# Optimization experiments

Hardware: AMD Instinct MI355X
Metric: run time of the kernel (lower is better)

## Reference

```python
import jax, jax.numpy as jnp
import numpy as np

N = 8192
D = 128
NUM_CLASSES = 1000
MARGIN = 1.0
EPS = 1e-6  # torch.nn.functional.pairwise_distance default eps
FMAX = float(np.finfo(np.float32).max)


def setup_inputs() -> dict:
    key = jax.random.key(0)
    k_e, k_l = jax.random.split(key)
    embed = jax.random.normal(k_e, (N, D), dtype=jnp.float32)
    labels = jax.random.randint(k_l, (N,), 0, NUM_CLASSES, dtype=jnp.int64)
    return {"embed": embed, "labels": labels}


def reference(embed, labels):
    # Pairwise squared-L2 distance matrix: ||xi||^2 - 2 xi.xj + ||xj||^2  -> [N, N]
    norm_sq = jnp.sum(embed * embed, axis=1, keepdims=True)  # [N, 1]
    dist = norm_sq - 2.0 * (embed @ embed.T) + norm_sq.T     # [N, N]

    # Label similarity mask (int in original; float here for the multiplies)
    sim = (labels[:, None] == labels[None, :]).astype(dist.dtype)  # [N, N]

    # Hardest positive: argmax of masked distances
    hardest_pos = jnp.argmax(dist * sim, axis=1)  # [N]

    # Hardest negative: argmin over negatives, sentinel-replacing masked-out entries
    neg_masked = dist * (1.0 - sim)
    hardest_neg = jnp.argmin(neg_masked + (neg_masked <= 0).astype(dist.dtype) * FMAX, axis=1)

    a = embed
    p = embed[hardest_pos]  # [N, D]
    n = embed[hardest_neg]  # [N, D]

    # torch.nn.TripletMarginLoss(margin=MARGIN): mean(relu(d(a,p) - d(a,n) + margin))
    # with d(x, y) = ||x - y + eps||_2 (torch pairwise_distance semantics)
    d_ap = jnp.sqrt(jnp.sum((a - p + EPS) ** 2, axis=1))
    d_an = jnp.sqrt(jnp.sum((a - n + EPS) ** 2, axis=1))
    loss = jnp.mean(jnp.maximum(d_ap - d_an + MARGIN, 0.0))
    return loss
```

## Files before the change

### kernel.cpp

```cpp
#include <hip/hip_runtime.h>
#include <cstdint>

typedef unsigned long long u64;
typedef _Float16 half8 __attribute__((ext_vector_type(8)));
typedef float f32x4 __attribute__((ext_vector_type(4)));

static constexpr int Dd = 128;
static constexpr float EPSf = 1e-6f;
static constexpr float MARGINf = 1.0f;
static constexpr float BIGf = 3.0e38f;

__device__ __forceinline__ unsigned fkey(float f) {
  unsigned b = __float_as_uint(f);
  return (b & 0x80000000u) ? ~b : (b | 0x80000000u);
}

__global__ __launch_bounds__(256) void k_prep(const float* __restrict__ E,
                                              const int* __restrict__ lab,
                                              _Float16* __restrict__ Eh,
                                              float2* __restrict__ nl,
                                              u64* __restrict__ posPack,
                                              u64* __restrict__ negPack) {
  int row = (blockIdx.x * 256 + threadIdx.x) >> 6;
  int l = threadIdx.x & 63;
  float2 v = *(const float2*)(E + row * Dd + l * 2);
  union { _Float16 h[2]; unsigned u; } cv;
  cv.h[0] = (_Float16)v.x;
  cv.h[1] = (_Float16)v.y;
  *(unsigned*)(Eh + row * Dd + l * 2) = cv.u;
  float s = v.x * v.x + v.y * v.y;
  #pragma unroll
  for (int off = 32; off; off >>= 1) s += __shfl_xor(s, off);
  if (l == 0) {
    float2 q;
    q.x = s;
    q.y = __int_as_float(lab[row]);
    nl[row] = q;
    posPack[row] = 0ull;
    negPack[row] = ~0ull;
  }
}

__global__ __launch_bounds__(512, 2) void k_gemm(const _Float16* __restrict__ Eh,
                                                 const float2* __restrict__ nl,
                                                 const int* __restrict__ lab,
                                                 u64* __restrict__ posPack,
                                                 u64* __restrict__ negPack) {
  __shared__ __align__(1024) _Float16 As[256 * 128];
  __shared__ __align__(1024) _Float16 Bs[256 * 128];
  __shared__ __align__(16) float2 nlj[256];

  const int t = threadIdx.x;
  const int w = t >> 6, l = t & 63;
  const int jbase = (blockIdx.x >> 5) * 256;
  const int ibase = (blockIdx.x & 31) * 256;
  const int lane15 = l & 15, lg = l >> 4;
  const int iw = w & 3, jw = w >> 2;

  {
    const int cp = lane15 << 4;
    #pragma unroll
    for (int ci = 0; ci < 16; ++ci) {
      int chunk = w * 16 + ci;
      int r = (chunk & 63) * 4 + lg;
      int gbase = (chunk < 64) ? jbase : ibase;
      _Float16* tile = (chunk < 64) ? As : Bs;
      half8 v = *(const half8*)((const char*)Eh + (size_t)(gbase + r) * 256 + cp);
      *(half8*)((char*)tile + r * 256 + (cp ^ ((r & 7) << 4))) = v;
    }
    if (t < 256) nlj[t] = nl[jbase + t];
  }

  int li[4];
  #pragma unroll
  for (int it = 0; it < 4; ++it) li[it] = lab[ibase + iw * 64 + it * 16 + lane15];

  __syncthreads();

  f32x4 acc[8][4];
  #pragma unroll
  for (int a = 0; a < 8; ++a)
    #pragma unroll
    for (int b = 0; b < 4; ++b) acc[a][b] = (f32x4){0.f, 0.f, 0.f, 0.f};

  #pragma unroll
  for (int ks = 0; ks < 4; ++ks) {
    const int bc = ks * 64 + lg * 16;
    half8 af[8], bf[4];
    #pragma unroll
    for (int jt = 0; jt < 8; ++jt) {
      int r = jw * 128 + jt * 16 + lane15;
      af[jt] = *(const half8*)((const char*)As + r * 256 + (bc ^ ((r & 7) << 4)));
    }
    #pragma unroll
    for (int it = 0; it < 4; ++it) {
      int r = iw * 64 + it * 16 + lane15;
      bf[it] = *(const half8*)((const char*)Bs + r * 256 + (bc ^ ((r & 7) << 4)));
    }
    #pragma unroll
    for (int jt = 0; jt < 8; ++jt)
      #pragma unroll
      for (int it = 0; it < 4; ++it)
        acc[jt][it] = __builtin_amdgcn_mfma_f32_16x16x32_f16(af[jt], bf[it], acc[jt][it], 0, 0, 0);
  }

  float bp[4], bn[4];
  #pragma unroll
  for (int it = 0; it < 4; ++it) { bp[it] = -BIGf; bn[it] = BIGf; }

  #pragma unroll
  for (int jt = 0; jt < 8; ++jt) {
    const int jr0 = jw * 128 + jt * 16 + lg * 4;
    float4 q01 = *(const float4*)(nlj + jr0);
    float4 q23 = *(const float4*)(nlj + jr0 + 2);
    float nj[4] = {q01.x, q01.z, q23.x, q23.z};
    int ljv[4] = {__float_as_int(q01.y), __float_as_int(q01.w),
                  __float_as_int(q23.y), __float_as_int(q23.w)};
    #pragma unroll
    for (int it = 0; it < 4; ++it) {
      float pc[4], nc[4];
      #pragma unroll
      for (int r = 0; r < 4; ++r) {
        float d = fmaf(acc[jt][it][r], -2.0f, nj[r]);
        float dv = __uint_as_float((__float_as_uint(d) & 0xFFFFFF00u) |
                                   (unsigned)(jr0 + r));
        bool sim = (ljv[r] == li[it]);
        pc[r] = sim ? dv : -BIGf;
        nc[r] = sim ? BIGf : dv;
      }
      bp[it] = fmaxf(bp[it], fmaxf(fmaxf(pc[0], pc[1]), fmaxf(pc[2], pc[3])));
      bn[it] = fminf(bn[it], fminf(fminf(nc[0], nc[1]), fminf(nc[2], nc[3])));
    }
  }

  #pragma unroll
  for (int it = 0; it < 4; ++it) {
    #pragma unroll
    for (int s = 16; s < 64; s <<= 1) {
      bp[it] = fmaxf(bp[it], __shfl_xor(bp[it], s));
      bn[it] = fminf(bn[it], __shfl_xor(bn[it], s));
    }
  }
  if (l < 16) {
    #pragma unroll
    for (int it = 0; it < 4; ++it) {
      int gi = ibase + iw * 64 + it * 16 + lane15;
      int jp = jbase + (int)(__float_as_uint(bp[it]) & 255u);
      int jn = jbase + (int)(__float_as_uint(bn[it]) & 255u);
      atomicMax(posPack + gi, ((u64)fkey(bp[it]) << 32) | (u64)(0xFFFFFFFFu - (unsigned)jp));
      atomicMin(negPack + gi, ((u64)fkey(bn[it]) << 32) | (u64)(unsigned)jn);
    }
  }
}

__global__ __launch_bounds__(256) void k_final(const float* __restrict__ E,
                                               const u64* __restrict__ posPack,
                                               const u64* __restrict__ negPack,
                                               float* __restrict__ rowLoss) {
  int i = (blockIdx.x * 256 + threadIdx.x) >> 6;
  int l = threadIdx.x & 63;
  int jp = (int)(0xFFFFFFFFu - (unsigned)(posPack[i] & 0xFFFFFFFFull));
  int jn = (int)(unsigned)(negPack[i] & 0xFFFFFFFFull);
  float2 a = *(const float2*)(E + i * Dd + l * 2);
  float2 p = *(const float2*)(E + jp * Dd + l * 2);
  float2 n = *(const float2*)(E + jn * Dd + l * 2);
  float dx = a.x - p.x + EPSf, dy = a.y - p.y + EPSf;
  float sap = dx * dx + dy * dy;
  dx = a.x - n.x + EPSf;
  dy = a.y - n.y + EPSf;
  float san = dx * dx + dy * dy;
  #pragma unroll
  for (int off = 32; off; off >>= 1) {
    sap += __shfl_xor(sap, off);
    san += __shfl_xor(san, off);
  }
  if (l == 0) rowLoss[i] = fmaxf(sqrtf(sap) - sqrtf(san) + MARGINf, 0.0f);
}

__global__ __launch_bounds__(256) void k_reduce(const float* __restrict__ rowLoss,
                                                float* __restrict__ out) {
  __shared__ float s[256];
  int t = threadIdx.x;
  float sum = 0.f;
  for (int q = 0; q < 32; ++q) sum += rowLoss[t + 256 * q];
  s[t] = sum;
  __syncthreads();
  for (int off = 128; off; off >>= 1) {
    if (t < off) s[t] += s[t + off];
    __syncthreads();
  }
  if (t == 0) out[0] = s[0] * (1.0f / 8192.0f);
}

extern "C" void kernel_launch(void* const* d_in, const int* in_sizes, int n_in,
                              void* d_out, int out_size, void* d_ws, size_t ws_size,
                              hipStream_t stream) {
  const float* E = (const float*)d_in[0];
  const int* lab = (const int*)d_in[1];
  float* out = (float*)d_out;

  char* wsp = (char*)d_ws;
  u64* posPack = (u64*)wsp;
  u64* negPack = (u64*)(wsp + (64 << 10));
  float2* nl = (float2*)(wsp + (128 << 10));
  float* rowLoss = (float*)(wsp + (192 << 10));
  _Float16* Eh = (_Float16*)(wsp + (256 << 10));

  k_prep<<<2048, 256, 0, stream>>>(E, lab, Eh, nl, posPack, negPack);
  k_gemm<<<1024, 512, 0, stream>>>(Eh, nl, lab, posPack, negPack);
  k_final<<<2048, 256, 0, stream>>>(E, posPack, negPack, rowLoss);
  k_reduce<<<1, 256, 0, stream>>>(rowLoss, out);
}
```

Baseline: 49.14 us.

## Stream j-tiles with double-buffered direct-to-LDS loads and drop global atomics

The GEMM kernel now assigns each block a 128-row i-tile against a 1024-column j-strip. The i fragments stay in registers while four 256-row j-tiles are streamed through double-buffered LDS using global_load_lds, so the next tile's loads overlap the current tile's MFMAs. Per-block argmax/argmin results go to per-strip partial arrays instead of 64-bit atomics, and the final kernel reduces over the 8 strips. This cuts LDS staging cost and atomic contention, at the price of fewer blocks (512) and a larger workspace. The distance value now keeps fewer mantissa bits because 10 bits are used to hold the column index.

```diff
diff --git a/kernel.cpp b/kernel.cpp
--- a/kernel.cpp
+++ b/kernel.cpp
@@ -15,12 +15,16 @@
   return (b & 0x80000000u) ? ~b : (b | 0x80000000u);
 }
 
+__device__ __forceinline__ void gl_lds16(const void* g, void* l) {
+  __builtin_amdgcn_global_load_lds(
+      (const __attribute__((address_space(1))) unsigned int*)g,
+      (__attribute__((address_space(3))) unsigned int*)l, 16, 0, 0);
+}
+
 __global__ __launch_bounds__(256) void k_prep(const float* __restrict__ E,
                                               const int* __restrict__ lab,
                                               _Float16* __restrict__ Eh,
-                                              float2* __restrict__ nl,
-                                              u64* __restrict__ posPack,
-                                              u64* __restrict__ negPack) {
+                                              float2* __restrict__ nl) {
   int row = (blockIdx.x * 256 + threadIdx.x) >> 6;
   int l = threadIdx.x & 63;
   float2 v = *(const float2*)(E + row * Dd + l * 2);
@@ -36,101 +40,133 @@
     q.x = s;
     q.y = __int_as_float(lab[row]);
     nl[row] = q;
-    posPack[row] = 0ull;
-    negPack[row] = ~0ull;
   }
 }
 
 __global__ __launch_bounds__(512, 2) void k_gemm(const _Float16* __restrict__ Eh,
                                                  const float2* __restrict__ nl,
                                                  const int* __restrict__ lab,
-                                                 u64* __restrict__ posPack,
-                                                 u64* __restrict__ negPack) {
-  __shared__ __align__(1024) _Float16 As[256 * 128];
-  __shared__ __align__(1024) _Float16 Bs[256 * 128];
-  __shared__ __align__(16) float2 nlj[256];
+                                                 u64* __restrict__ posPart,
+                                                 u64* __restrict__ negPart) {
+  __shared__ __align__(16) _Float16 jA[2][256 * 128];
+  __shared__ __align__(16) float2 jNL[2][256];
+  __shared__ float sc[2][4][128];
 
   const int t = threadIdx.x;
   const int w = t >> 6, l = t & 63;
-  const int jbase = (blockIdx.x >> 5) * 256;
-  const int ibase = (blockIdx.x & 31) * 256;
   const int lane15 = l & 15, lg = l >> 4;
-  const int iw = w & 3, jw = w >> 2;
-
-  {
-    const int cp = lane15 << 4;
-    #pragma unroll
-    for (int ci = 0; ci < 16; ++ci) {
-      int chunk = w * 16 + ci;
-      int r = (chunk & 63) * 4 + lg;
-      int gbase = (chunk < 64) ? jbase : ibase;
-      _Float16* tile = (chunk < 64) ? As : Bs;
-      half8 v = *(const half8*)((const char*)Eh + (size_t)(gbase + r) * 256 + cp);
-      *(half8*)((char*)tile + r * 256 + (cp ^ ((r & 7) << 4))) = v;
-    }
-    if (t < 256) nlj[t] = nl[jbase + t];
-  }
+  const int ig = w & 1, jw = w >> 1;
+  const int ip = blockIdx.x & 63, js = blockIdx.x >> 6;
+  const int ibase = ip * 128;
+  const int jbase = js * 1024;
+
+  #pragma unroll
+  for (int qi = 0; qi < 4; ++qi) {
+    int q = w * 4 + qi;
+    int row = q * 4 + lg;
+    gl_lds16((const char*)Eh + (size_t)(ibase + row) * 256 + ((lane15 << 4) ^ ((row & 7) << 4)),
+             (char*)&jA[0][0] + q * 1024);
+  }
+  #pragma unroll
+  for (int qi = 0; qi < 8; ++qi) {
+    int q = w * 8 + qi;
+    int row = q * 4 + lg;
+    gl_lds16((const char*)Eh + (size_t)(jbase + row) * 256 + ((lane15 << 4) ^ ((row & 7) << 4)),
+             (char*)&jA[1][0] + q * 1024);
+  }
+  if (w < 2)
+    gl_lds16((const char*)nl + (size_t)jbase * 8 + w * 1024 + l * 16,
+             (char*)&jNL[1][0] + w * 1024);
 
   int li[4];
   #pragma unroll
-  for (int it = 0; it < 4; ++it) li[it] = lab[ibase + iw * 64 + it * 16 + lane15];
-
-  __syncthreads();
-
-  f32x4 acc[8][4];
-  #pragma unroll
-  for (int a = 0; a < 8; ++a)
-    #pragma unroll
-    for (int b = 0; b < 4; ++b) acc[a][b] = (f32x4){0.f, 0.f, 0.f, 0.f};
-
-  #pragma unroll
-  for (int ks = 0; ks < 4; ++ks) {
-    const int bc = ks * 64 + lg * 16;
-    half8 af[8], bf[4];
-    #pragma unroll
-    for (int jt = 0; jt < 8; ++jt) {
-      int r = jw * 128 + jt * 16 + lane15;
-      af[jt] = *(const half8*)((const char*)As + r * 256 + (bc ^ ((r & 7) << 4)));
-    }
-    #pragma unroll
-    for (int it = 0; it < 4; ++it) {
-      int r = iw * 64 + it * 16 + lane15;
-      bf[it] = *(const half8*)((const char*)Bs + r * 256 + (bc ^ ((r & 7) << 4)));
-    }
-    #pragma unroll
-    for (int jt = 0; jt < 8; ++jt)
-      #pragma unroll
-      for (int it = 0; it < 4; ++it)
-        acc[jt][it] = __builtin_amdgcn_mfma_f32_16x16x32_f16(af[jt], bf[it], acc[jt][it], 0, 0, 0);
-  }
+  for (int it = 0; it < 4; ++it) li[it] = lab[ibase + ig * 64 + it * 16 + lane15];
+
+  __syncthreads();
+
+  half8 bf[4][4];
+  #pragma unroll
+  for (int it = 0; it < 4; ++it) {
+    #pragma unroll
+    for (int ks = 0; ks < 4; ++ks) {
+      int r = ig * 64 + it * 16 + lane15;
+      int bc = ks * 64 + lg * 16;
+      bf[it][ks] = *(const half8*)((const char*)&jA[0][0] + r * 256 + (bc ^ ((r & 7) << 4)));
+    }
+  }
+  __syncthreads();
 
   float bp[4], bn[4];
   #pragma unroll
   for (int it = 0; it < 4; ++it) { bp[it] = -BIGf; bn[it] = BIGf; }
 
   #pragma unroll
-  for (int jt = 0; jt < 8; ++jt) {
-    const int jr0 = jw * 128 + jt * 16 + lg * 4;
-    float4 q01 = *(const float4*)(nlj + jr0);
-    float4 q23 = *(const float4*)(nlj + jr0 + 2);
-    float nj[4] = {q01.x, q01.z, q23.x, q23.z};
-    int ljv[4] = {__float_as_int(q01.y), __float_as_int(q01.w),
-                  __float_as_int(q23.y), __float_as_int(q23.w)};
-    #pragma unroll
-    for (int it = 0; it < 4; ++it) {
-      float pc[4], nc[4];
-      #pragma unroll
-      for (int r = 0; r < 4; ++r) {
-        float d = fmaf(acc[jt][it][r], -2.0f, nj[r]);
-        float dv = __uint_as_float((__float_as_uint(d) & 0xFFFFFF00u) |
-                                   (unsigned)(jr0 + r));
-        bool sim = (ljv[r] == li[it]);
-        pc[r] = sim ? dv : -BIGf;
-        nc[r] = sim ? BIGf : dv;
+  for (int tt = 0; tt < 4; ++tt) {
+    const int cur = 1 - (tt & 1);
+    const int nxt = tt & 1;
+
+    if (tt < 3) {
+      const int jr = jbase + (tt + 1) * 256;
+      #pragma unroll
+      for (int qi = 0; qi < 8; ++qi) {
+        int q = w * 8 + qi;
+        int row = q * 4 + lg;
+        gl_lds16((const char*)Eh + (size_t)(jr + row) * 256 + ((lane15 << 4) ^ ((row & 7) << 4)),
+                 (char*)&jA[nxt][0] + q * 1024);
       }
-      bp[it] = fmaxf(bp[it], fmaxf(fmaxf(pc[0], pc[1]), fmaxf(pc[2], pc[3])));
-      bn[it] = fminf(bn[it], fminf(fminf(nc[0], nc[1]), fminf(nc[2], nc[3])));
-    }
+      if (w < 2)
+        gl_lds16((const char*)nl + (size_t)jr * 8 + w * 1024 + l * 16,
+                 (char*)&jNL[nxt][0] + w * 1024);
+    }
+
+    f32x4 acc[4][4];
+    #pragma unroll
+    for (int a = 0; a < 4; ++a)
+      #pragma unroll
+      for (int b = 0; b < 4; ++b) acc[a][b] = (f32x4){0.f, 0.f, 0.f, 0.f};
+
+    #pragma unroll
+    for (int ks = 0; ks < 4; ++ks) {
+      const int bc = ks * 64 + lg * 16;
+      half8 af[4];
+      #pragma unroll
+      for (int jt = 0; jt < 4; ++jt) {
+        int r = jw * 64 + jt * 16 + lane15;
+        af[jt] = *(const half8*)((const char*)&jA[cur][0] + r * 256 + (bc ^ ((r & 7) << 4)));
+      }
+      #pragma unroll
+      for (int jt = 0; jt < 4; ++jt)
+        #pragma unroll
+        for (int it = 0; it < 4; ++it)
+          acc[jt][it] = __builtin_amdgcn_mfma_f32_16x16x32_f16(af[jt], bf[it][ks], acc[jt][it], 0, 0, 0);
+    }
+
+    const unsigned tb = (unsigned)(tt * 256 + jw * 64 + lg * 4);
+    #pragma unroll
+    for (int jt = 0; jt < 4; ++jt) {
+      const int jr0 = jw * 64 + jt * 16 + lg * 4;
+      float4 q01 = *(const float4*)&jNL[cur][jr0];
+      float4 q23 = *(const float4*)&jNL[cur][jr0 + 2];
+      const float njv[4] = {q01.x, q01.z, q23.x, q23.z};
+      const int ljv[4] = {__float_as_int(q01.y), __float_as_int(q01.w),
+                          __float_as_int(q23.y), __float_as_int(q23.w)};
+      const unsigned ib = tb + (unsigned)(jt * 16);
+      #pragma unroll
+      for (int it = 0; it < 4; ++it) {
+        float pcv[4], ncv[4];
+        #pragma unroll
+        for (int r = 0; r < 4; ++r) {
+          float d = fmaf(acc[jt][it][r], -2.0f, njv[r]);
+          float dv = __uint_as_float((__float_as_uint(d) & 0xFFFFFC00u) | (ib + (unsigned)r));
+          bool sim = (ljv[r] == li[it]);
+          pcv[r] = sim ? dv : -BIGf;
+          ncv[r] = sim ? BIGf : dv;
+        }
+        bp[it] = fmaxf(bp[it], fmaxf(fmaxf(pcv[0], pcv[1]), fmaxf(pcv[2], pcv[3])));
+        bn[it] = fminf(bn[it], fminf(fminf(ncv[0], ncv[1]), fminf(ncv[2], ncv[3])));
+      }
+    }
+    __syncthreads();
   }
 
   #pragma unroll
@@ -144,23 +180,39 @@
   if (l < 16) {
     #pragma unroll
     for (int it = 0; it < 4; ++it) {
-      int gi = ibase + iw * 64 + it * 16 + lane15;
-      int jp = jbase + (int)(__float_as_uint(bp[it]) & 255u);
-      int jn = jbase + (int)(__float_as_uint(bn[it]) & 255u);
-      atomicMax(posPack + gi, ((u64)fkey(bp[it]) << 32) | (u64)(0xFFFFFFFFu - (unsigned)jp));
-      atomicMin(negPack + gi, ((u64)fkey(bn[it]) << 32) | (u64)(unsigned)jn);
-    }
+      sc[0][jw][ig * 64 + it * 16 + lane15] = bp[it];
+      sc[1][jw][ig * 64 + it * 16 + lane15] = bn[it];
+    }
+  }
+  __syncthreads();
+
+  if (t < 128) {
+    float p = fmaxf(fmaxf(sc[0][0][t], sc[0][1][t]), fmaxf(sc[0][2][t], sc[0][3][t]));
+    float n = fminf(fminf(sc[1][0][t], sc[1][1][t]), fminf(sc[1][2][t], sc[1][3][t]));
+    unsigned jp = (unsigned)jbase + (__float_as_uint(p) & 1023u);
+    unsigned jn = (unsigned)jbase + (__float_as_uint(n) & 1023u);
+    posPart[(size_t)js * 8192 + ibase + t] =
+        ((u64)fkey(p) << 32) | (u64)(0xFFFFFFFFu - jp);
+    negPart[(size_t)js * 8192 + ibase + t] = ((u64)fkey(n) << 32) | (u64)jn;
   }
 }
 
 __global__ __launch_bounds__(256) void k_final(const float* __restrict__ E,
-                                               const u64* __restrict__ posPack,
-                                               const u64* __restrict__ negPack,
+                                               const u64* __restrict__ posPart,
+                                               const u64* __restrict__ negPart,
                                                float* __restrict__ rowLoss) {
   int i = (blockIdx.x * 256 + threadIdx.x) >> 6;
   int l = threadIdx.x & 63;
-  int jp = (int)(0xFFFFFFFFu - (unsigned)(posPack[i] & 0xFFFFFFFFull));
-  int jn = (int)(unsigned)(negPack[i] & 0xFFFFFFFFull);
+  u64 pp = 0ull, np = ~0ull;
+  #pragma unroll
+  for (int s = 0; s < 8; ++s) {
+    u64 a = posPart[(size_t)s * 8192 + i];
+    u64 b = negPart[(size_t)s * 8192 + i];
+    pp = pp > a ? pp : a;
+    np = np < b ? np : b;
+  }
+  int jp = (int)(0xFFFFFFFFu - (unsigned)(pp & 0xFFFFFFFFull));
+  int jn = (int)(unsigned)(np & 0xFFFFFFFFull);
   float2 a = *(const float2*)(E + i * Dd + l * 2);
   float2 p = *(const float2*)(E + jp * Dd + l * 2);
   float2 n = *(const float2*)(E + jn * Dd + l * 2);
@@ -200,14 +252,14 @@
   float* out = (float*)d_out;
 
   char* wsp = (char*)d_ws;
-  u64* posPack = (u64*)wsp;
-  u64* negPack = (u64*)(wsp + (64 << 10));
-  float2* nl = (float2*)(wsp + (128 << 10));
-  float* rowLoss = (float*)(wsp + (192 << 10));
-  _Float16* Eh = (_Float16*)(wsp + (256 << 10));
-
-  k_prep<<<2048, 256, 0, stream>>>(E, lab, Eh, nl, posPack, negPack);
-  k_gemm<<<1024, 512, 0, stream>>>(Eh, nl, lab, posPack, negPack);
-  k_final<<<2048, 256, 0, stream>>>(E, posPack, negPack, rowLoss);
+  u64* posPart = (u64*)wsp;
+  u64* negPart = (u64*)(wsp + (512 << 10));
+  float2* nl = (float2*)(wsp + (1024 << 10));
+  float* rowLoss = (float*)(wsp + (1088 << 10));
+  _Float16* Eh = (_Float16*)(wsp + (1152 << 10));
+
+  k_prep<<<2048, 256, 0, stream>>>(E, lab, Eh, nl);
+  k_gemm<<<512, 512, 0, stream>>>(Eh, nl, lab, posPart, negPart);
+  k_final<<<2048, 256, 0, stream>>>(E, posPart, negPart, rowLoss);
   k_reduce<<<1, 256, 0, stream>>>(rowLoss, out);
 }
```

Measured after the change: 48.06 us. 1.02x faster.

## Pre-pack fp16 embeddings in MFMA fragment layout and shrink GEMM tiles to 128x128

Applied to the files above, without the earlier changes.

The prep kernel now writes the fp16 embeddings in a layout that matches the MFMA fragment order, so the GEMM can copy tiles to LDS linearly and read fragments without the XOR swizzle. The GEMM block tile drops from 256x256 with 512 threads to 128x128 with 256 threads, which gives four times as many blocks and fewer accumulators per wave. It also raises wave priority around the MFMA sequence. The cost is more redundant tile loads across blocks and more atomic updates, and the packed index now keeps only 7 low bits, which slightly changes how near-tied distances are broken.

```diff
diff --git a/kernel.cpp b/kernel.cpp
--- a/kernel.cpp
+++ b/kernel.cpp
@@ -16,139 +16,140 @@
 }
 
 __global__ __launch_bounds__(256) void k_prep(const float* __restrict__ E,
-                                              const int* __restrict__ lab,
-                                              _Float16* __restrict__ Eh,
-                                              float2* __restrict__ nl,
+                                              _Float16* __restrict__ Ehp,
+                                              float* __restrict__ normf,
                                               u64* __restrict__ posPack,
                                               u64* __restrict__ negPack) {
-  int row = (blockIdx.x * 256 + threadIdx.x) >> 6;
-  int l = threadIdx.x & 63;
-  float2 v = *(const float2*)(E + row * Dd + l * 2);
-  union { _Float16 h[2]; unsigned u; } cv;
-  cv.h[0] = (_Float16)v.x;
-  cv.h[1] = (_Float16)v.y;
-  *(unsigned*)(Eh + row * Dd + l * 2) = cv.u;
-  float s = v.x * v.x + v.y * v.y;
-  #pragma unroll
-  for (int off = 32; off; off >>= 1) s += __shfl_xor(s, off);
-  if (l == 0) {
-    float2 q;
-    q.x = s;
-    q.y = __int_as_float(lab[row]);
-    nl[row] = q;
+  __shared__ float part[4][16];
+  const int t = threadIdx.x;
+  const int b = blockIdx.x;
+  const int ks = t >> 6, r15 = t & 15;
+  const int lg = (t >> 4) & 3;
+  const float* src = E + (size_t)(b * 16 + r15) * Dd + ks * 32 + lg * 8;
+  float4 v0 = *(const float4*)src;
+  float4 v1 = *(const float4*)(src + 4);
+  half8 hv;
+  hv[0] = (_Float16)v0.x; hv[1] = (_Float16)v0.y;
+  hv[2] = (_Float16)v0.z; hv[3] = (_Float16)v0.w;
+  hv[4] = (_Float16)v1.x; hv[5] = (_Float16)v1.y;
+  hv[6] = (_Float16)v1.z; hv[7] = (_Float16)v1.w;
+  *(half8*)((char*)Ehp + (size_t)b * 4096 + t * 16) = hv;
+  float s = v0.x * v0.x + v0.y * v0.y + v0.z * v0.z + v0.w * v0.w +
+            v1.x * v1.x + v1.y * v1.y + v1.z * v1.z + v1.w * v1.w;
+  s += __shfl_xor(s, 16);
+  s += __shfl_xor(s, 32);
+  if (((t >> 4) & 3) == 0) part[ks][r15] = s;
+  __syncthreads();
+  if (t < 16) {
+    int row = b * 16 + t;
+    normf[row] = part[0][t] + part[1][t] + part[2][t] + part[3][t];
     posPack[row] = 0ull;
     negPack[row] = ~0ull;
   }
 }
 
-__global__ __launch_bounds__(512, 2) void k_gemm(const _Float16* __restrict__ Eh,
-                                                 const float2* __restrict__ nl,
+__global__ __launch_bounds__(256, 2) void k_gemm(const _Float16* __restrict__ Ehp,
+                                                 const float* __restrict__ normf,
                                                  const int* __restrict__ lab,
                                                  u64* __restrict__ posPack,
                                                  u64* __restrict__ negPack) {
-  __shared__ __align__(1024) _Float16 As[256 * 128];
-  __shared__ __align__(1024) _Float16 Bs[256 * 128];
-  __shared__ __align__(16) float2 nlj[256];
+  __shared__ __align__(16) char As[32768];
+  __shared__ __align__(16) char Bs[32768];
+  __shared__ __align__(16) float njs[128];
+  __shared__ __align__(16) int ljs[128];
 
   const int t = threadIdx.x;
   const int w = t >> 6, l = t & 63;
-  const int jbase = (blockIdx.x >> 5) * 256;
-  const int ibase = (blockIdx.x & 31) * 256;
   const int lane15 = l & 15, lg = l >> 4;
-  const int iw = w & 3, jw = w >> 2;
-
-  {
-    const int cp = lane15 << 4;
-    #pragma unroll
-    for (int ci = 0; ci < 16; ++ci) {
-      int chunk = w * 16 + ci;
-      int r = (chunk & 63) * 4 + lg;
-      int gbase = (chunk < 64) ? jbase : ibase;
-      _Float16* tile = (chunk < 64) ? As : Bs;
-      half8 v = *(const half8*)((const char*)Eh + (size_t)(gbase + r) * 256 + cp);
-      *(half8*)((char*)tile + r * 256 + (cp ^ ((r & 7) << 4))) = v;
-    }
-    if (t < 256) nlj[t] = nl[jbase + t];
-  }
-
+  const int iw = w & 1, jw = w >> 1;
+  const int ibase = (blockIdx.x & 63) * 128;
+  const int jbase = (blockIdx.x >> 6) * 128;
+  const char* jsrc = (const char*)Ehp + (size_t)(jbase >> 4) * 4096;
+  const char* isrc = (const char*)Ehp + (size_t)(ibase >> 4) * 4096;
+
+  #pragma unroll
+  for (int p = 0; p < 8; ++p)
+    *(half8*)(As + p * 4096 + t * 16) = *(const half8*)(jsrc + p * 4096 + t * 16);
+  #pragma unroll
+  for (int p = 0; p < 8; ++p)
+    *(half8*)(Bs + p * 4096 + t * 16) = *(const half8*)(isrc + p * 4096 + t * 16);
+  if (t < 128) {
+    njs[t] = normf[jbase + t];
+    ljs[t] = lab[jbase + t];
+  }
   int li[4];
   #pragma unroll
   for (int it = 0; it < 4; ++it) li[it] = lab[ibase + iw * 64 + it * 16 + lane15];
-
   __syncthreads();
 
-  f32x4 acc[8][4];
-  #pragma unroll
-  for (int a = 0; a < 8; ++a)
+  f32x4 acc[4][4];
+  #pragma unroll
+  for (int a = 0; a < 4; ++a)
     #pragma unroll
     for (int b = 0; b < 4; ++b) acc[a][b] = (f32x4){0.f, 0.f, 0.f, 0.f};
 
   #pragma unroll
   for (int ks = 0; ks < 4; ++ks) {
-    const int bc = ks * 64 + lg * 16;
-    half8 af[8], bf[4];
-    #pragma unroll
-    for (int jt = 0; jt < 8; ++jt) {
-      int r = jw * 128 + jt * 16 + lane15;
-      af[jt] = *(const half8*)((const char*)As + r * 256 + (bc ^ ((r & 7) << 4)));
-    }
-    #pragma unroll
-    for (int it = 0; it < 4; ++it) {
-      int r = iw * 64 + it * 16 + lane15;
-      bf[it] = *(const half8*)((const char*)Bs + r * 256 + (bc ^ ((r & 7) << 4)));
-    }
-    #pragma unroll
-    for (int jt = 0; jt < 8; ++jt)
+    half8 af[4], bf[4];
+    #pragma unroll
+    for (int jt = 0; jt < 4; ++jt)
+      af[jt] = *(const half8*)(As + ((jw * 4 + jt) * 4 + ks) * 1024 + l * 16);
+    #pragma unroll
+    for (int it = 0; it < 4; ++it)
+      bf[it] = *(const half8*)(Bs + ((iw * 4 + it) * 4 + ks) * 1024 + l * 16);
+    __builtin_amdgcn_s_setprio(1);
+    #pragma unroll
+    for (int jt = 0; jt < 4; ++jt)
       #pragma unroll
       for (int it = 0; it < 4; ++it)
         acc[jt][it] = __builtin_amdgcn_mfma_f32_16x16x32_f16(af[jt], bf[it], acc[jt][it], 0, 0, 0);
-  }
-
-  float bp[4], bn[4];
-  #pragma unroll
-  for (int it = 0; it < 4; ++it) { bp[it] = -BIGf; bn[it] = BIGf; }
-
-  #pragma unroll
-  for (int jt = 0; jt < 8; ++jt) {
-    const int jr0 = jw * 128 + jt * 16 + lg * 4;
-    float4 q01 = *(const float4*)(nlj + jr0);
-    float4 q23 = *(const float4*)(nlj + jr0 + 2);
-    float nj[4] = {q01.x, q01.z, q23.x, q23.z};
-    int ljv[4] = {__float_as_int(q01.y), __float_as_int(q01.w),
-                  __float_as_int(q23.y), __float_as_int(q23.w)};
+    __builtin_amdgcn_s_setprio(0);
+  }
+
+  float bp[4] = {-BIGf, -BIGf, -BIGf, -BIGf};
+  float bn[4] = {BIGf, BIGf, BIGf, BIGf};
+
+  #pragma unroll
+  for (int jt = 0; jt < 4; ++jt) {
+    const int jr0 = jw * 64 + jt * 16 + lg * 4;
+    const float4 nj4 = *(const float4*)&njs[jr0];
+    const int4 lj4 = *(const int4*)&ljs[jr0];
     #pragma unroll
     for (int it = 0; it < 4; ++it) {
-      float pc[4], nc[4];
-      #pragma unroll
-      for (int r = 0; r < 4; ++r) {
-        float d = fmaf(acc[jt][it][r], -2.0f, nj[r]);
-        float dv = __uint_as_float((__float_as_uint(d) & 0xFFFFFF00u) |
-                                   (unsigned)(jr0 + r));
-        bool sim = (ljv[r] == li[it]);
-        pc[r] = sim ? dv : -BIGf;
-        nc[r] = sim ? BIGf : dv;
-      }
-      bp[it] = fmaxf(bp[it], fmaxf(fmaxf(pc[0], pc[1]), fmaxf(pc[2], pc[3])));
-      bn[it] = fminf(bn[it], fminf(fminf(nc[0], nc[1]), fminf(nc[2], nc[3])));
+      float c0 = fmaf(acc[jt][it][0], -2.0f, nj4.x);
+      float c1 = fmaf(acc[jt][it][1], -2.0f, nj4.y);
+      float c2 = fmaf(acc[jt][it][2], -2.0f, nj4.z);
+      float c3 = fmaf(acc[jt][it][3], -2.0f, nj4.w);
+      c0 = __uint_as_float((__float_as_uint(c0) & 0xFFFFFF80u) | (unsigned)(jr0 + 0));
+      c1 = __uint_as_float((__float_as_uint(c1) & 0xFFFFFF80u) | (unsigned)(jr0 + 1));
+      c2 = __uint_as_float((__float_as_uint(c2) & 0xFFFFFF80u) | (unsigned)(jr0 + 2));
+      c3 = __uint_as_float((__float_as_uint(c3) & 0xFFFFFF80u) | (unsigned)(jr0 + 3));
+      bool s0 = (lj4.x == li[it]), s1 = (lj4.y == li[it]);
+      bool s2 = (lj4.z == li[it]), s3 = (lj4.w == li[it]);
+      float p0 = s0 ? c0 : -BIGf, p1 = s1 ? c1 : -BIGf;
+      float p2 = s2 ? c2 : -BIGf, p3 = s3 ? c3 : -BIGf;
+      float n0 = s0 ? BIGf : c0, n1 = s1 ? BIGf : c1;
+      float n2 = s2 ? BIGf : c2, n3 = s3 ? BIGf : c3;
+      bp[it] = fmaxf(bp[it], fmaxf(fmaxf(p0, p1), fmaxf(p2, p3)));
+      bn[it] = fminf(bn[it], fminf(fminf(n0, n1), fminf(n2, n3)));
     }
   }
 
   #pragma unroll
   for (int it = 0; it < 4; ++it) {
-    #pragma unroll
-    for (int s = 16; s < 64; s <<= 1) {
-      bp[it] = fmaxf(bp[it], __shfl_xor(bp[it], s));
-      bn[it] = fminf(bn[it], __shfl_xor(bn[it], s));
-    }
+    bp[it] = fmaxf(bp[it], __shfl_xor(bp[it], 16));
+    bp[it] = fmaxf(bp[it], __shfl_xor(bp[it], 32));
+    bn[it] = fminf(bn[it], __shfl_xor(bn[it], 16));
+    bn[it] = fminf(bn[it], __shfl_xor(bn[it], 32));
   }
   if (l < 16) {
     #pragma unroll
     for (int it = 0; it < 4; ++it) {
       int gi = ibase + iw * 64 + it * 16 + lane15;
-      int jp = jbase + (int)(__float_as_uint(bp[it]) & 255u);
-      int jn = jbase + (int)(__float_as_uint(bn[it]) & 255u);
-      atomicMax(posPack + gi, ((u64)fkey(bp[it]) << 32) | (u64)(0xFFFFFFFFu - (unsigned)jp));
-      atomicMin(negPack + gi, ((u64)fkey(bn[it]) << 32) | (u64)(unsigned)jn);
+      unsigned gjp = (unsigned)jbase + (__float_as_uint(bp[it]) & 127u);
+      unsigned gjn = (unsigned)jbase + (__float_as_uint(bn[it]) & 127u);
+      atomicMax(posPack + gi, ((u64)fkey(bp[it]) << 32) | (u64)(0xFFFFFFFFu - gjp));
+      atomicMin(negPack + gi, ((u64)fkey(bn[it]) << 32) | (u64)gjn);
     }
   }
 }
@@ -161,9 +162,9 @@
   int l = threadIdx.x & 63;
   int jp = (int)(0xFFFFFFFFu - (unsigned)(posPack[i] & 0xFFFFFFFFull));
   int jn = (int)(unsigned)(negPack[i] & 0xFFFFFFFFull);
-  float2 a = *(const float2*)(E + i * Dd + l * 2);
-  float2 p = *(const float2*)(E + jp * Dd + l * 2);
-  float2 n = *(const float2*)(E + jn * Dd + l * 2);
+  float2 a = *(const float2*)(E + (size_t)i * Dd + l * 2);
+  float2 p = *(const float2*)(E + (size_t)jp * Dd + l * 2);
+  float2 n = *(const float2*)(E + (size_t)jn * Dd + l * 2);
   float dx = a.x - p.x + EPSf, dy = a.y - p.y + EPSf;
   float sap = dx * dx + dy * dy;
   dx = a.x - n.x + EPSf;
@@ -202,12 +203,12 @@
   char* wsp = (char*)d_ws;
   u64* posPack = (u64*)wsp;
   u64* negPack = (u64*)(wsp + (64 << 10));
-  float2* nl = (float2*)(wsp + (128 << 10));
-  float* rowLoss = (float*)(wsp + (192 << 10));
-  _Float16* Eh = (_Float16*)(wsp + (256 << 10));
-
-  k_prep<<<2048, 256, 0, stream>>>(E, lab, Eh, nl, posPack, negPack);
-  k_gemm<<<1024, 512, 0, stream>>>(Eh, nl, lab, posPack, negPack);
+  float* normf = (float*)(wsp + (128 << 10));
+  float* rowLoss = (float*)(wsp + (160 << 10));
+  _Float16* Ehp = (_Float16*)(wsp + (192 << 10));
+
+  k_prep<<<512, 256, 0, stream>>>(E, Ehp, normf, posPack, negPack);
+  k_gemm<<<4096, 256, 0, stream>>>(Ehp, normf, lab, posPack, negPack);
   k_final<<<2048, 256, 0, stream>>>(E, posPack, negPack, rowLoss);
   k_reduce<<<1, 256, 0, stream>>>(rowLoss, out);
 }
```

New measurement: 54.20 us. 10.3% more time.
